# Optimization experiments

Measured on AMD Instinct MI355X. Metric: run time of the kernel, lower is better.

The kernel has to match this reference:

```python
import jax, jax.numpy as jnp
from jax import lax
import numpy as np

B, C, T = 128, 9, 512
M = 64                 # fourier modes
D_OB = 40
D_MODEL = C * D_OB     # 360
D_PE = 16
D = D_MODEL + D_PE     # 376
NHEAD = 4
DH = D // NHEAD        # 94
NHID = 2 * D_MODEL     # 720
NLAYERS = 3
FRAC = 0.5
MAX_PE = 100.0
EPS = 1e-5

def setup_inputs() -> dict:
    key = jax.random.key(0)
    ks = jax.random.split(key, 16)
    scale = 1.0 / (C * C)
    f32 = jnp.float32
    return {
        "x": jax.random.normal(ks[0], (B, C, T), f32),
        "w1r": scale * jax.random.uniform(ks[1], (C, C, M), f32),
        "w1i": scale * jax.random.uniform(ks[2], (C, C, M), f32),
        "conv_w": 0.1 * jax.random.normal(ks[3], (1, C, 3), f32),
        "bnf_g": jnp.ones((2 * M,), f32), "bnf_b": jnp.zeros((2 * M,), f32),
        "R_u": 1.0 + 0.02 * jax.random.normal(ks[4], (D_MODEL,), f32),
        "Wg1": 0.1 * jax.random.normal(ks[5], (D_OB, D_OB), f32),
        "Wg2": 0.1 * jax.random.normal(ks[6], (D_OB, D_OB), f32),
        "Wqkv": 0.02 * jax.random.normal(ks[7], (NLAYERS, D, 3 * D), f32),
        "bqkv": jnp.zeros((NLAYERS, 3 * D), f32),
        "Wo": 0.02 * jax.random.normal(ks[8], (NLAYERS, D, D), f32),
        "bo": jnp.zeros((NLAYERS, D), f32),
        "ln1g": jnp.ones((NLAYERS, D), f32), "ln1b": jnp.zeros((NLAYERS, D), f32),
        "W1": 0.02 * jax.random.normal(ks[9], (NLAYERS, D, NHID), f32),
        "b1": jnp.zeros((NLAYERS, NHID), f32),
        "W2": 0.02 * jax.random.normal(ks[10], (NLAYERS, NHID, D), f32),
        "b2": jnp.zeros((NLAYERS, D), f32),
        "ln2g": jnp.ones((NLAYERS, D), f32), "ln2b": jnp.zeros((NLAYERS, D), f32),
        "Wp": 0.02 * jax.random.normal(ks[11], (D, T), f32),
        "bp": jnp.zeros((T,), f32),
        "bnp_g": jnp.ones((T,), f32), "bnp_b": jnp.zeros((T,), f32),
    }

def _layernorm(z, g, b):
    m = z.mean(-1, keepdims=True)
    v = ((z - m) ** 2).mean(-1, keepdims=True)
    return (z - m) * lax.rsqrt(v + EPS) * g + b

def _batchnorm(z, g, b):  # training-mode BN over batch dim, z: [N, F]
    m = z.mean(0)
    v = ((z - m) ** 2).mean(0)
    return (z - m) * lax.rsqrt(v + EPS) * g + b

def _forward(x, w1r, w1i, conv_w, bnf_g, bnf_b, R_u, Wg1, Wg2,
             Wqkv, bqkv, Wo, bo, ln1g, ln1b, W1, b1, W2, b2, ln2g, ln2b,
             Wp, bp, bnp_g, bnp_b):
    # ---- SpectralConv1d (FrFT branch) ----
    xc = jnp.cos(x)                                   # [B,C,T]
    k = jnp.arange(T, dtype=jnp.float32)
    chirp = jnp.exp(-1j * jnp.pi * FRAC * k * k / T)  # FrFT chirp
    x_frft = jnp.fft.ifft(jnp.fft.fft(xc) * chirp)    # [B,C,T] complex
    w1 = (w1r + 1j * w1i).astype(jnp.complex64)
    out_modes = jnp.einsum('bix,iox->box', x_frft[:, :, :M], w1)   # [B,C,M]
    out_ft = jnp.concatenate([out_modes, jnp.zeros((B, C, T - M), jnp.complex64)], -1)
    ef = jnp.concatenate([jnp.abs(out_modes), jnp.angle(out_modes)], -1)  # [B,C,2M]
    # avg: Conv1d(C->1, k=3, pad=1, stride=1, no bias), then squeeze
    ef = lax.conv_general_dilated(ef, conv_w, window_strides=(1,), padding=((1, 1),),
                                  dimension_numbers=('NCH', 'OIH', 'NCH'))[:, 0, :]  # [B,2M]
    ef = jax.nn.relu(_batchnorm(ef, bnf_g, bnf_b))
    # ---- Raindrop branch ----
    src = jnp.transpose(x, (2, 0, 1))                 # [T,B,C]
    h = jnp.repeat(src, D_OB, axis=-1)                # repeat_interleave -> [T,B,d_model]
    h = jax.nn.relu(h * R_u)
    h4 = h.reshape(T, B, C, D_OB)
    adj = jnp.full((C, C), 1.0 / C, x.dtype)          # global_structure = ones, normalized
    h4 = jax.nn.relu(jnp.einsum('mn,tbnd,de->tbme', adj, h4, Wg1))
    h4 = jax.nn.relu(jnp.einsum('mn,tbnd,de->tbme', adj, h4, Wg2))
    h = h4.reshape(T, B, D_MODEL)
    # time positional encoding (PositionalEncodingTF, d_pe=16, MAX=100)
    times = jnp.broadcast_to(jnp.arange(T, dtype=jnp.float32)[:, None], (T, B))
    timescales = jnp.power(MAX_PE, jnp.linspace(0.0, 1.0, D_PE // 2))
    st = times[:, :, None] / timescales               # [T,B,8]
    pe = jnp.concatenate([jnp.sin(st), jnp.cos(st)], -1)  # [T,B,16]
    z = jnp.concatenate([h, pe], -1).transpose(1, 0, 2)   # [B,T,D]
    inv_sqrt_dh = 1.0 / np.sqrt(DH).astype(np.float32)
    for l in range(NLAYERS):
        qkv = z @ Wqkv[l] + bqkv[l]
        q, kk, v = jnp.split(qkv, 3, axis=-1)
        hd = lambda t: t.reshape(B, T, NHEAD, DH).transpose(0, 2, 1, 3)
        q, kk, v = hd(q), hd(kk), hd(v)
        att = jax.nn.softmax(jnp.einsum('bhqd,bhkd->bhqk', q, kk) * inv_sqrt_dh, axis=-1)
        o = jnp.einsum('bhqk,bhkd->bhqd', att, v).transpose(0, 2, 1, 3).reshape(B, T, D)
        z = _layernorm(z + o @ Wo[l] + bo[l], ln1g[l], ln1b[l])
        ff = jax.nn.relu(z @ W1[l] + b1[l]) @ W2[l] + b2[l]
        z = _layernorm(z + ff, ln2g[l], ln2b[l])
    et = z.mean(axis=1)                               # 'mean' aggregation -> [B,D]
    # projection: Linear(D, T) + ReLU + BatchNorm1d(T)
    et = _batchnorm(jax.nn.relu(et @ Wp + bp), bnp_g, bnp_b)  # [B,T]
    f = jnp.concatenate([ef, et], -1)                 # [B, 2M+T]
    fn = f / jnp.maximum(jnp.linalg.norm(f, axis=-1, keepdims=True), 1e-12)
    return fn, out_ft

def reference(x, w1r, w1i, conv_w, bnf_g, bnf_b, R_u, Wg1, Wg2,
              Wqkv, bqkv, Wo, bo, ln1g, ln1b, W1, b1, W2, b2, ln2g, ln2b,
              Wp, bp, bnp_g, bnp_b):
    return _forward(x, w1r, w1i, conv_w, bnf_g, bnf_b, R_u, Wg1, Wg2,
                    Wqkv, bqkv, Wo, bo, ln1g, ln1b, W1, b1, W2, b2, ln2g, ln2b,
                    Wp, bp, bnp_g, bnp_b)
```

## Files before the change

kernel.cpp:

```cpp
#include <hip/hip_runtime.h>
#include <math.h>

constexpr int cB = 128;
constexpr int cC = 9;
constexpr int cT = 512;
constexpr int cM = 64;
constexpr int cDOB = 40;
constexpr int cDM = 360;
constexpr int cD = 376;
constexpr int cDH = 94;
constexpr int cNHID = 720;
constexpr float cEPS = 1e-5f;
constexpr float cPI = 3.14159265358979323846f;

typedef __attribute__((ext_vector_type(8))) short short8b;
typedef __attribute__((ext_vector_type(4))) float f32x4;

__device__ __forceinline__ short f2b(float f) {
  union { float f; unsigned u; } c; c.f = f;
  unsigned r = (c.u + 0x7fffu + ((c.u >> 16) & 1u)) >> 16;
  return (short)r;
}
__device__ __forceinline__ float b2f(short h) {
  union { unsigned u; float f; } c; c.u = ((unsigned)(unsigned short)h) << 16;
  return c.f;
}

__global__ void k_chirp(float2* __restrict__ g) {
  int d = threadIdx.x;
  float re = 0.f, im = 0.f;
  for (int k = 0; k < cT; ++k) {
    int q = (k * k) & 2047;
    int p = (k * d) & 511;
    float th = cPI * ((float)p * (1.0f / 256.0f) - (float)q * (1.0f / 1024.0f));
    float s, c;
    sincosf(th, &s, &c);
    re += c; im += s;
  }
  g[d] = make_float2(re * (1.0f / 512.0f), im * (1.0f / 512.0f));
}

__global__ __launch_bounds__(512) void k_spectral(
    const float* __restrict__ x, const float* __restrict__ w1r,
    const float* __restrict__ w1i, const float2* __restrict__ g,
    float* __restrict__ outft, float* __restrict__ EF) {
  __shared__ float xc[cC][cT];
  __shared__ float2 gs[cT];
  __shared__ float2 xfr[cC][cM];
  int b = blockIdx.x, tid = threadIdx.x;
  for (int i = tid; i < cC * cT; i += 512)
    xc[i / cT][i % cT] = cosf(x[(size_t)b * cC * cT + i]);
  for (int i = tid; i < cT; i += 512) gs[i] = g[i];
  __syncthreads();
  for (int idx = tid; idx < cC * cM; idx += 512) {
    int c = idx / cM, m = idx % cM;
    float re = 0.f, im = 0.f;
    for (int t = 0; t < cT; ++t) {
      float xv = xc[c][t];
      float2 gv = gs[(m - t) & (cT - 1)];
      re += xv * gv.x; im += xv * gv.y;
    }
    xfr[c][m] = make_float2(re, im);
  }
  __syncthreads();
  for (int idx = tid; idx < cC * cM; idx += 512) {
    int o = idx / cM, m = idx % cM;
    float re = 0.f, im = 0.f;
    #pragma unroll
    for (int i = 0; i < cC; ++i) {
      float2 xv = xfr[i][m];
      float wr = w1r[(i * cC + o) * cM + m];
      float wi = w1i[(i * cC + o) * cM + m];
      re += xv.x * wr - xv.y * wi;
      im += xv.x * wi + xv.y * wr;
    }
    outft[(size_t)(b * cC + o) * cT + m] = re;
    EF[(b * cC + o) * (2 * cM) + m] = sqrtf(re * re + im * im);
    EF[(b * cC + o) * (2 * cM) + cM + m] = atan2f(im, re);
  }
  for (int idx = tid; idx < cC * (cT - cM); idx += 512) {
    int o = idx / (cT - cM);
    int r = idx % (cT - cM);
    outft[(size_t)(b * cC + o) * cT + cM + r] = 0.f;
  }
}

__global__ void k_convef(const float* __restrict__ EF, const float* __restrict__ cw,
                         float* __restrict__ efp) {
  int i = blockIdx.x * blockDim.x + threadIdx.x;
  if (i >= cB * 2 * cM) return;
  int b = i / (2 * cM), f = i % (2 * cM);
  float acc = 0.f;
  #pragma unroll
  for (int c = 0; c < cC; ++c) {
    const float* row = EF + (b * cC + c) * (2 * cM);
    if (f > 0) acc += row[f - 1] * cw[c * 3 + 0];
    acc += row[f] * cw[c * 3 + 1];
    if (f < 2 * cM - 1) acc += row[f + 1] * cw[c * 3 + 2];
  }
  efp[i] = acc;
}

__global__ __launch_bounds__(128) void k_bn(const float* __restrict__ in,
    const float* __restrict__ gam, const float* __restrict__ bet,
    float* __restrict__ dst, int F, int stride, int off, int reluAfter) {
  __shared__ float red[128];
  int f = blockIdx.x, bt = threadIdx.x;
  float v = in[(size_t)bt * F + f];
  red[bt] = v; __syncthreads();
  for (int s = 64; s > 0; s >>= 1) { if (bt < s) red[bt] += red[bt + s]; __syncthreads(); }
  float mean = red[0] * (1.0f / 128.0f);
  __syncthreads();
  float d = v - mean;
  red[bt] = d * d; __syncthreads();
  for (int s = 64; s > 0; s >>= 1) { if (bt < s) red[bt] += red[bt + s]; __syncthreads(); }
  float var = red[0] * (1.0f / 128.0f);
  float o = d * rsqrtf(var + cEPS) * gam[f] + bet[f];
  if (reluAfter) o = fmaxf(o, 0.f);
  dst[(size_t)bt * stride + off + f] = o;
}

__global__ __launch_bounds__(256) void k_raindrop(const float* __restrict__ x,
    const float* __restrict__ Ru, const float* __restrict__ Wg1,
    const float* __restrict__ Wg2, float* __restrict__ Z,
    short* __restrict__ Zb16, int bStart) {
  __shared__ float w1s[cDOB * cDOB], w2s[cDOB * cDOB], rus[cDM], tss[8];
  __shared__ float vsh[256][cDOB];
  int tid = threadIdx.x;
  for (int i = tid; i < cDOB * cDOB; i += 256) { w1s[i] = Wg1[i]; w2s[i] = Wg2[i]; }
  for (int i = tid; i < cDM; i += 256) rus[i] = Ru[i];
  if (tid < 8) tss[tid] = powf(100.0f, (float)tid * (1.0f / 7.0f));
  __syncthreads();
  int token0 = blockIdx.x * 256;
  int token = token0 + tid;
  int bl = token / cT, t = token % cT;
  int bg = bStart + bl;
  float s[cDOB];
  #pragma unroll
  for (int d = 0; d < cDOB; ++d) s[d] = 0.f;
  #pragma unroll
  for (int c = 0; c < cC; ++c) {
    float xv = x[((size_t)bg * cC + c) * cT + t];
    #pragma unroll
    for (int d = 0; d < cDOB; ++d) s[d] += fmaxf(xv * rus[c * cDOB + d], 0.f);
  }
  #pragma unroll
  for (int d = 0; d < cDOB; ++d) s[d] *= (1.0f / 9.0f);
  float u[cDOB];
  #pragma unroll
  for (int e = 0; e < cDOB; ++e) {
    float a = 0.f;
    #pragma unroll
    for (int d = 0; d < cDOB; ++d) a += s[d] * w1s[d * cDOB + e];
    u[e] = fmaxf(a, 0.f);
  }
  #pragma unroll
  for (int e = 0; e < cDOB; ++e) {
    float a = 0.f;
    #pragma unroll
    for (int d = 0; d < cDOB; ++d) a += u[d] * w2s[d * cDOB + e];
    vsh[tid][e] = fmaxf(a, 0.f);
  }
  __syncthreads();
  size_t zbase = (size_t)token0 * cD;
  for (int i = tid; i < 256 * cD; i += 256) {
    int tok = i / cD, col = i % cD;
    float val;
    if (col < cDM) {
      val = vsh[tok][col % cDOB];
    } else {
      int j = col - cDM;
      int tt = (token0 + tok) % cT;
      float st = (float)tt / tss[j & 7];
      val = (j < 8) ? sinf(st) : cosf(st);
    }
    Z[zbase + i] = val;
    Zb16[zbase + i] = f2b(val);
  }
}

__global__ __launch_bounds__(256) void k_cvtT(const float* __restrict__ in,
    short* __restrict__ out, int K, int N) {
  __shared__ float tile[32][33];
  int kb = blockIdx.x * 32, nb = blockIdx.y * 32;
  int tx = threadIdx.x & 31, ty = threadIdx.x >> 5;
  for (int i = ty; i < 32; i += 8) {
    int k = kb + i, n = nb + tx;
    tile[i][tx] = (k < K && n < N) ? in[(size_t)k * N + n] : 0.f;
  }
  __syncthreads();
  for (int i = ty; i < 32; i += 8) {
    int n = nb + i, k = kb + tx;
    if (n < N && k < K) out[(size_t)n * K + k] = f2b(tile[tx][i]);
  }
}

#define GEMM_CORE(EPILOGUE)                                                       \
  __shared__ short As[128][40];                                                   \
  __shared__ short Bs[128][40];                                                   \
  int tid = threadIdx.x;                                                          \
  int nbx = gridDim.x;                                                            \
  int flat = blockIdx.y * nbx + blockIdx.x;                                       \
  int nwg = nbx * gridDim.y;                                                      \
  int swz = ((nwg & 7) == 0) ? ((flat & 7) * (nwg >> 3) + (flat >> 3)) : flat;    \
  int m0 = (swz / nbx) * 128, n0 = (swz % nbx) * 128;                             \
  int w = tid >> 6, l = tid & 63;                                                 \
  int wm = w >> 1, wn = w & 1;                                                    \
  int lr = l & 15, lg = l >> 4;                                                   \
  f32x4 acc[4][4];                                                                \
  _Pragma("unroll") for (int i = 0; i < 4; ++i)                                   \
    _Pragma("unroll") for (int j = 0; j < 4; ++j)                                 \
      _Pragma("unroll") for (int r = 0; r < 4; ++r) acc[i][j][r] = 0.f;           \
  int srow = tid >> 1, skq = (tid & 1) << 4;                                      \
  int nK = (Kd + 31) >> 5;                                                        \
  for (int ks = 0; ks < nK; ++ks) {                                               \
    int k0 = ks << 5;                                                             \
    {                                                                             \
      int gm = m0 + srow;                                                         \
      int gk = k0 + skq;                                                          \
      short tmp[16];                                                              \
      const short* ap = At + (size_t)gm * Kd + gk;                                \
      _Pragma("unroll") for (int c = 0; c < 2; ++c) {                             \
        if (gm < Mr && gk + c * 8 + 7 < Kd) {                                     \
          *(short8b*)&tmp[c * 8] = *(const short8b*)(ap + c * 8);                 \
        } else {                                                                  \
          _Pragma("unroll") for (int j = 0; j < 8; ++j) tmp[c * 8 + j] = (short)0;\
        }                                                                         \
      }                                                                           \
      *(short8b*)&As[srow][skq]     = *(short8b*)&tmp[0];                         \
      *(short8b*)&As[srow][skq + 8] = *(short8b*)&tmp[8];                         \
    }                                                                             \
    {                                                                             \
      int gn = n0 + srow;                                                         \
      int gk = k0 + skq;                                                          \
      short tmp[16];                                                              \
      const short* bp = Bt + (size_t)gn * Kd + gk;                                \
      _Pragma("unroll") for (int c = 0; c < 2; ++c) {                             \
        if (gn < Nc && gk + c * 8 + 7 < Kd) {                                     \
          *(short8b*)&tmp[c * 8] = *(const short8b*)(bp + c * 8);                 \
        } else {                                                                  \
          _Pragma("unroll") for (int j = 0; j < 8; ++j) tmp[c * 8 + j] = (short)0;\
        }                                                                         \
      }                                                                           \
      *(short8b*)&Bs[srow][skq]     = *(short8b*)&tmp[0];                         \
      *(short8b*)&Bs[srow][skq + 8] = *(short8b*)&tmp[8];                         \
    }                                                                             \
    __syncthreads();                                                              \
    short8b af[4], bf[4];                                                         \
    _Pragma("unroll") for (int i = 0; i < 4; ++i)                                 \
      af[i] = *(short8b*)&As[wm * 64 + i * 16 + lr][lg * 8];                      \
    _Pragma("unroll") for (int j = 0; j < 4; ++j)                                 \
      bf[j] = *(short8b*)&Bs[wn * 64 + j * 16 + lr][lg * 8];                      \
    _Pragma("unroll") for (int i = 0; i < 4; ++i)                                 \
      _Pragma("unroll") for (int j = 0; j < 4; ++j)                               \
        acc[i][j] = __builtin_amdgcn_mfma_f32_16x16x32_bf16(af[i], bf[j], acc[i][j], 0, 0, 0); \
    __syncthreads();                                                              \
  }                                                                               \
  _Pragma("unroll") for (int i = 0; i < 4; ++i)                                   \
    _Pragma("unroll") for (int j = 0; j < 4; ++j) {                               \
      int gn = n0 + wn * 64 + j * 16 + lr;                                        \
      if (gn >= Nc) continue;                                                     \
      float bv = bias ? bias[gn] : 0.f;                                           \
      int gmb = m0 + wm * 64 + i * 16 + lg * 4;                                   \
      _Pragma("unroll") for (int r = 0; r < 4; ++r) {                             \
        int gm = gmb + r;                                                         \
        if (gm >= Mr) continue;                                                   \
        float vv = acc[i][j][r] + bv;                                             \
        EPILOGUE                                                                  \
      }                                                                           \
    }

__global__ __launch_bounds__(256) void k_gemm_mfma2(
    const short* __restrict__ At, const short* __restrict__ Bt,
    const float* __restrict__ bias, float* __restrict__ Cm,
    int Mr, int Nc, int Kd, int relu) {
  GEMM_CORE({
    if (relu) vv = fmaxf(vv, 0.f);
    Cm[(size_t)gm * Nc + gn] = vv;
  })
}

__global__ __launch_bounds__(256) void k_gemm_b16(
    const short* __restrict__ At, const short* __restrict__ Bt,
    const float* __restrict__ bias, short* __restrict__ Cm,
    int Mr, int Nc, int Kd, int relu) {
  GEMM_CORE({
    if (relu) vv = fmaxf(vv, 0.f);
    Cm[(size_t)gm * Nc + gn] = f2b(vv);
  })
}

__global__ __launch_bounds__(256) void k_gemm_qkv(
    const short* __restrict__ At, const short* __restrict__ Bt,
    const float* __restrict__ bias, unsigned* __restrict__ Cp,
    int Mr, int Nc, int Kd) {
  GEMM_CORE({
    short hv = f2b(vv);
    short lv2 = f2b(vv - b2f(hv));
    Cp[(size_t)gm * Nc + gn] =
        ((unsigned)(unsigned short)hv) | (((unsigned)(unsigned short)lv2) << 16);
  })
}

__global__ __launch_bounds__(256) void k_gemm(const float* __restrict__ A,
    const float* __restrict__ Bm, const float* __restrict__ bias,
    float* __restrict__ Cm, int Mr, int Nc, int Kd, int relu) {
  __shared__ float As[16][68];
  __shared__ float Bs[16][68];
  int tid = threadIdx.x;
  int tx = tid & 15, ty = tid >> 4;
  int n0 = blockIdx.x * 64, m0 = blockIdx.y * 64;
  float acc[4][4] = {{0.f}};
  for (int k0 = 0; k0 < Kd; k0 += 16) {
    {
      int row = tid >> 2, kq = (tid & 3) << 2;
      int gm = m0 + row, gk = k0 + kq;
      float4 av = make_float4(0.f, 0.f, 0.f, 0.f);
      if (gm < Mr) {
        const float* ap = A + (size_t)gm * Kd + gk;
        if (gk + 3 < Kd) av = *(const float4*)ap;
        else {
          if (gk + 0 < Kd) av.x = ap[0];
          if (gk + 1 < Kd) av.y = ap[1];
          if (gk + 2 < Kd) av.z = ap[2];
        }
      }
      As[kq + 0][row] = av.x; As[kq + 1][row] = av.y;
      As[kq + 2][row] = av.z; As[kq + 3][row] = av.w;
    }
    {
      int kr = tid >> 4, nc = (tid & 15) << 2;
      int gk = k0 + kr, gn = n0 + nc;
      float4 bv = make_float4(0.f, 0.f, 0.f, 0.f);
      if (gk < Kd && gn < Nc) {
        const float* bp = Bm + (size_t)gk * Nc + gn;
        if (gn + 3 < Nc) bv = *(const float4*)bp;
        else {
          bv.x = bp[0];
          if (gn + 1 < Nc) bv.y = bp[1];
          if (gn + 2 < Nc) bv.z = bp[2];
        }
      }
      *(float4*)&Bs[kr][nc] = bv;
    }
    __syncthreads();
    #pragma unroll
    for (int k = 0; k < 16; ++k) {
      float4 a = *(const float4*)&As[k][ty << 2];
      float4 b = *(const float4*)&Bs[k][tx << 2];
      acc[0][0] += a.x * b.x; acc[0][1] += a.x * b.y; acc[0][2] += a.x * b.z; acc[0][3] += a.x * b.w;
      acc[1][0] += a.y * b.x; acc[1][1] += a.y * b.y; acc[1][2] += a.y * b.z; acc[1][3] += a.y * b.w;
      acc[2][0] += a.z * b.x; acc[2][1] += a.z * b.y; acc[2][2] += a.z * b.z; acc[2][3] += a.z * b.w;
      acc[3][0] += a.w * b.x; acc[3][1] += a.w * b.y; acc[3][2] += a.w * b.z; acc[3][3] += a.w * b.w;
    }
    __syncthreads();
  }
  #pragma unroll
  for (int i = 0; i < 4; ++i) {
    int gm = m0 + (ty << 2) + i;
    if (gm >= Mr) continue;
    #pragma unroll
    for (int j = 0; j < 4; ++j) {
      int gn = n0 + (tx << 2) + j;
      if (gn >= Nc) continue;
      float v = acc[i][j] + (bias ? bias[gn] : 0.f);
      if (relu) v = fmaxf(v, 0.f);
      Cm[(size_t)gm * Nc + gn] = v;
    }
  }
}

__global__ __launch_bounds__(512) void k_attn_mfma2(const unsigned* __restrict__ Qp,
    short* __restrict__ ATT16) {
  __shared__ __align__(16) char raw[62464];
  short* kv_h = (short*)raw;
  short* kv_l = (short*)(raw + 12288);
  int tid = threadIdx.x;
  int w = tid >> 6, l = tid & 63;
  int lr = l & 15, lg = l >> 4;
  short* p_h = (short*)(raw + 24576) + w * 16 * 72;
  short* p_l = (short*)(raw + 43008) + w * 16 * 72;
  float* fs_w = (float*)(raw + 61440) + w * 16;
  float* il_w = (float*)(raw + 61952) + w * 16;
  int qb = blockIdx.x, h = blockIdx.y, bl = blockIdx.z;
  size_t tokBase = (size_t)bl * cT;
  const float scale = 0.103142125f;
  int qrow = w * 16 + lr;

  short8b qh_s[3], ql_s[3];
  #pragma unroll
  for (int ph = 0; ph < 2; ++ph) {
    size_t base = (tokBase + qb * 128 + ph * 64) * 1128ull + h * cDH;
    for (int task = tid; task < 768; task += 512) {
      int oct = task >> 6, tok = task & 63;
      size_t src = base + (size_t)tok * 1128 + oct * 8;
      uint4 a = *(const uint4*)(Qp + src);
      uint4 b = *(const uint4*)(Qp + src + 4);
      unsigned p[8] = {a.x, a.y, a.z, a.w, b.x, b.y, b.z, b.w};
      short hv[8], lv[8];
      #pragma unroll
      for (int i = 0; i < 8; ++i) { hv[i] = (short)(p[i] & 0xffffu); lv[i] = (short)(p[i] >> 16); }
      if (oct == 11) { hv[6] = 0; hv[7] = 0; lv[6] = 0; lv[7] = 0; }
      int dst = (oct * 64 + (tok ^ (oct & 7))) * 8;
      *(short8b*)&kv_h[dst] = *(short8b*)hv;
      *(short8b*)&kv_l[dst] = *(short8b*)lv;
    }
    __syncthreads();
    if ((w >> 2) == ph) {
      int tokl = qrow & 63;
      #pragma unroll
      for (int s = 0; s < 3; ++s) {
        int o = s * 4 + lg;
        int src = (o * 64 + (tokl ^ (o & 7))) * 8;
        qh_s[s] = *(short8b*)&kv_h[src];
        ql_s[s] = *(short8b*)&kv_l[src];
      }
    }
    __syncthreads();
  }

  f32x4 of[6];
  #pragma unroll
  for (int f = 0; f < 6; ++f)
    #pragma unroll
    for (int r = 0; r < 4; ++r) of[f][r] = 0.f;
  float mrow[4], lrow[4];
  #pragma unroll
  for (int r = 0; r < 4; ++r) { mrow[r] = -1e30f; lrow[r] = 0.f; }

  for (int kt = 0; kt < 8; ++kt) {
    __syncthreads();
    {
      size_t base = (tokBase + kt * 64) * 1128ull + cD + h * cDH;
      for (int task = tid; task < 768; task += 512) {
        int oct = task >> 6, tok = task & 63;
        size_t src = base + (size_t)tok * 1128 + oct * 8;
        uint4 a = *(const uint4*)(Qp + src);
        uint4 b = *(const uint4*)(Qp + src + 4);
        unsigned p[8] = {a.x, a.y, a.z, a.w, b.x, b.y, b.z, b.w};
        short hv[8], lv[8];
        #pragma unroll
        for (int i = 0; i < 8; ++i) { hv[i] = (short)(p[i] & 0xffffu); lv[i] = (short)(p[i] >> 16); }
        if (oct == 11) { hv[6] = 0; hv[7] = 0; lv[6] = 0; lv[7] = 0; }
        int dst = (oct * 64 + (tok ^ (oct & 7))) * 8;
        *(short8b*)&kv_h[dst] = *(short8b*)hv;
        *(short8b*)&kv_l[dst] = *(short8b*)lv;
      }
    }
    __syncthreads();
    f32x4 sf4[4];
    #pragma unroll
    for (int j = 0; j < 4; ++j)
      #pragma unroll
      for (int r = 0; r < 4; ++r) sf4[j][r] = 0.f;
    #pragma unroll
    for (int j = 0; j < 4; ++j) {
      #pragma unroll
      for (int s = 0; s < 3; ++s) {
        int o = s * 4 + lg;
        int src = (o * 64 + ((j * 16 + lr) ^ (o & 7))) * 8;
        short8b bh = *(short8b*)&kv_h[src];
        short8b bl2 = *(short8b*)&kv_l[src];
        sf4[j] = __builtin_amdgcn_mfma_f32_16x16x32_bf16(qh_s[s], bh, sf4[j], 0, 0, 0);
        sf4[j] = __builtin_amdgcn_mfma_f32_16x16x32_bf16(ql_s[s], bh, sf4[j], 0, 0, 0);
        sf4[j] = __builtin_amdgcn_mfma_f32_16x16x32_bf16(qh_s[s], bl2, sf4[j], 0, 0, 0);
      }
    }
    float fscv[4];
    #pragma unroll
    for (int r = 0; r < 4; ++r) {
      float s0 = sf4[0][r] * scale, s1 = sf4[1][r] * scale;
      float s2 = sf4[2][r] * scale, s3 = sf4[3][r] * scale;
      float mx = fmaxf(fmaxf(s0, s1), fmaxf(s2, s3));
      for (int off = 8; off > 0; off >>= 1) mx = fmaxf(mx, __shfl_xor(mx, off, 16));
      float mnew = fmaxf(mrow[r], mx);
      float fsc = __expf(mrow[r] - mnew);
      float p0 = __expf(s0 - mnew), p1 = __expf(s1 - mnew);
      float p2 = __expf(s2 - mnew), p3 = __expf(s3 - mnew);
      float ps = p0 + p1 + p2 + p3;
      for (int off = 8; off > 0; off >>= 1) ps += __shfl_xor(ps, off, 16);
      lrow[r] = lrow[r] * fsc + ps;
      mrow[r] = mnew;
      fscv[r] = fsc;
      int row = (lg * 4 + r) * 72;
      short h0 = f2b(p0);
      p_h[row + 0 * 16 + lr] = h0; p_l[row + 0 * 16 + lr] = f2b(p0 - b2f(h0));
      short h1 = f2b(p1);
      p_h[row + 1 * 16 + lr] = h1; p_l[row + 1 * 16 + lr] = f2b(p1 - b2f(h1));
      short h2 = f2b(p2);
      p_h[row + 2 * 16 + lr] = h2; p_l[row + 2 * 16 + lr] = f2b(p2 - b2f(h2));
      short h3 = f2b(p3);
      p_h[row + 3 * 16 + lr] = h3; p_l[row + 3 * 16 + lr] = f2b(p3 - b2f(h3));
    }
    if (lr == 0) {
      #pragma unroll
      for (int r = 0; r < 4; ++r) fs_w[lg * 4 + r] = fscv[r];
    }
    __syncthreads();
    {
      size_t base = (tokBase + kt * 64) * 1128ull + 2 * cD + h * cDH;
      for (int task = tid; task < 768; task += 512) {
        int d = task % 96, t8 = task / 96;
        short hv[8], lv[8];
        if (d < cDH) {
          #pragma unroll
          for (int i = 0; i < 8; ++i) {
            unsigned p = Qp[base + (size_t)(t8 * 8 + i) * 1128 + d];
            hv[i] = (short)(p & 0xffffu); lv[i] = (short)(p >> 16);
          }
        } else {
          #pragma unroll
          for (int i = 0; i < 8; ++i) { hv[i] = 0; lv[i] = 0; }
        }
        int dst = d * 64 + ((t8 * 8) ^ ((d & 7) << 3));
        *(short8b*)&kv_h[dst] = *(short8b*)hv;
        *(short8b*)&kv_l[dst] = *(short8b*)lv;
      }
    }
    __syncthreads();
    float fs = fs_w[lr];
    #pragma unroll
    for (int f = 0; f < 6; ++f)
      #pragma unroll
      for (int r = 0; r < 4; ++r) of[f][r] *= fs;
    #pragma unroll
    for (int s = 0; s < 2; ++s) {
      int pof = lr * 72 + s * 32 + lg * 8;
      short8b ph = *(short8b*)&p_h[pof];
      short8b pl = *(short8b*)&p_l[pof];
      #pragma unroll
      for (int f = 0; f < 6; ++f) {
        int d = f * 16 + lr;
        int vof = d * 64 + ((s * 32 + lg * 8) ^ ((d & 7) << 3));
        short8b vh = *(short8b*)&kv_h[vof];
        short8b vl = *(short8b*)&kv_l[vof];
        of[f] = __builtin_amdgcn_mfma_f32_16x16x32_bf16(vh, ph, of[f], 0, 0, 0);
        of[f] = __builtin_amdgcn_mfma_f32_16x16x32_bf16(vl, ph, of[f], 0, 0, 0);
        of[f] = __builtin_amdgcn_mfma_f32_16x16x32_bf16(vh, pl, of[f], 0, 0, 0);
      }
    }
  }
  if (lr == 0) {
    #pragma unroll
    for (int r = 0; r < 4; ++r) il_w[lg * 4 + r] = 1.0f / lrow[r];
  }
  __syncthreads();
  float il = il_w[lr];
  float* obuf = (float*)raw;
  #pragma unroll
  for (int f = 0; f < 6; ++f) {
    #pragma unroll
    for (int r = 0; r < 4; ++r) {
      int d = f * 16 + lg * 4 + r;
      if (d < cDH) obuf[(w * 16 + lr) * 98 + d] = of[f][r] * il;
    }
  }
  __syncthreads();
  for (int idx = tid; idx < 128 * cDH; idx += 512) {
    int q = idx / cDH, d = idx % cDH;
    ATT16[(tokBase + qb * 128 + q) * (size_t)cD + h * cDH + d] = f2b(obuf[q * 98 + d]);
  }
}

__global__ __launch_bounds__(256) void k_addln(float* __restrict__ Z,
    const float* __restrict__ Y, const float* __restrict__ gam,
    const float* __restrict__ bet, short* __restrict__ Zb16) {
  int wid = threadIdx.x >> 6, lane = threadIdx.x & 63;
  size_t base = ((size_t)blockIdx.x * 4 + wid) * cD;
  float v[6];
  float sum = 0.f;
  #pragma unroll
  for (int j = 0; j < 6; ++j) {
    int c = lane + j * 64;
    float t = 0.f;
    if (c < cD) t = Z[base + c] + Y[base + c];
    v[j] = t; sum += t;
  }
  #pragma unroll
  for (int off = 32; off > 0; off >>= 1) sum += __shfl_xor(sum, off, 64);
  float mean = sum / (float)cD;
  float vs = 0.f;
  #pragma unroll
  for (int j = 0; j < 6; ++j) {
    int c = lane + j * 64;
    if (c < cD) { float d = v[j] - mean; vs += d * d; }
  }
  #pragma unroll
  for (int off = 32; off > 0; off >>= 1) vs += __shfl_xor(vs, off, 64);
  float inv = rsqrtf(vs / (float)cD + cEPS);
  #pragma unroll
  for (int j = 0; j < 6; ++j) {
    int c = lane + j * 64;
    if (c < cD) {
      float res = (v[j] - mean) * inv * gam[c] + bet[c];
      Z[base + c] = res;
      Zb16[base + c] = f2b(res);
    }
  }
}

__global__ __launch_bounds__(384) void k_meant(const float* __restrict__ Z,
    float* __restrict__ et, int bStart) {
  int bl = blockIdx.x, d = threadIdx.x;
  if (d >= cD) return;
  float s = 0.f;
  for (int t = 0; t < cT; ++t) s += Z[((size_t)bl * cT + t) * cD + d];
  et[(size_t)(bStart + bl) * cD + d] = s * (1.0f / 512.0f);
}

__global__ __launch_bounds__(128) void k_final(const float* __restrict__ fst,
    float* __restrict__ out) {
  __shared__ float red[128];
  int b = blockIdx.x, tid = threadIdx.x;
  float v[5]; float ss = 0.f;
  #pragma unroll
  for (int i = 0; i < 5; ++i) {
    v[i] = fst[(size_t)b * 640 + tid + i * 128];
    ss += v[i] * v[i];
  }
  red[tid] = ss; __syncthreads();
  for (int s = 64; s > 0; s >>= 1) { if (tid < s) red[tid] += red[tid + s]; __syncthreads(); }
  float inv = 1.0f / fmaxf(sqrtf(red[0]), 1e-12f);
  #pragma unroll
  for (int i = 0; i < 5; ++i) out[(size_t)b * 640 + tid + i * 128] = v[i] * inv;
}

extern "C" void kernel_launch(void* const* d_in, const int* in_sizes, int n_in,
                              void* d_out, int out_size, void* d_ws, size_t ws_size,
                              hipStream_t stream) {
  (void)in_sizes; (void)n_in; (void)out_size;
  const float* x     = (const float*)d_in[0];
  const float* w1r   = (const float*)d_in[1];
  const float* w1i   = (const float*)d_in[2];
  const float* convw = (const float*)d_in[3];
  const float* bnfg  = (const float*)d_in[4];
  const float* bnfb  = (const float*)d_in[5];
  const float* Ru    = (const float*)d_in[6];
  const float* Wg1   = (const float*)d_in[7];
  const float* Wg2   = (const float*)d_in[8];
  const float* Wqkv  = (const float*)d_in[9];
  const float* bqkv  = (const float*)d_in[10];
  const float* Wo    = (const float*)d_in[11];
  const float* bo    = (const float*)d_in[12];
  const float* ln1g  = (const float*)d_in[13];
  const float* ln1b  = (const float*)d_in[14];
  const float* W1    = (const float*)d_in[15];
  const float* b1    = (const float*)d_in[16];
  const float* W2    = (const float*)d_in[17];
  const float* b2    = (const float*)d_in[18];
  const float* ln2g  = (const float*)d_in[19];
  const float* ln2b  = (const float*)d_in[20];
  const float* Wp    = (const float*)d_in[21];
  const float* bp    = (const float*)d_in[22];
  const float* bnpg  = (const float*)d_in[23];
  const float* bnpb  = (const float*)d_in[24];

  float* W = (float*)d_ws;
  size_t wsFloats = ws_size / 4;
  float* fst = W;
  float* et  = fst + 81920;
  float* etp = et + 48128;
  float2* g  = (float2*)(etp + 65536);
  float* EF  = (float*)g + 1024;
  float* efp = EF + 147456;
  short* bfw = (short*)(efp + 16384);
  const size_t bfwFloats = 1660416;
  const size_t fixedFloats = 81920 + 48128 + 65536 + 1024 + 147456 + 16384 + bfwFloats;

  const size_t oQKV = 0;
  const size_t oWO  = oQKV + (size_t)3 * 1128 * 376;
  const size_t oW1  = oWO  + (size_t)3 * 376 * 376;
  const size_t oW2  = oW1  + (size_t)3 * 720 * 376;

  float* outF  = (float*)d_out;
  float* outft = outF + cB * 640;

  if (wsFloats < fixedFloats) return;

  int Bc = 0;
  float* chunk = nullptr;
  for (int c = 128; c >= 1; c >>= 1) {
    size_t need = (size_t)c * cT * 1880 + 64;
    if (fixedFloats + need <= wsFloats) { Bc = c; chunk = W + fixedFloats; break; }
  }
  bool haveChunk = (Bc > 0);

  if (haveChunk) {
    for (int l = 0; l < 3; ++l) {
      k_cvtT<<<dim3(12, 36), 256, 0, stream>>>(Wqkv + (size_t)l * cD * 1128,
          bfw + oQKV + (size_t)l * 1128 * 376, cD, 1128);
      k_cvtT<<<dim3(12, 12), 256, 0, stream>>>(Wo + (size_t)l * cD * cD,
          bfw + oWO + (size_t)l * 376 * 376, cD, cD);
      k_cvtT<<<dim3(12, 23), 256, 0, stream>>>(W1 + (size_t)l * cD * cNHID,
          bfw + oW1 + (size_t)l * 720 * 376, cD, cNHID);
      k_cvtT<<<dim3(23, 12), 256, 0, stream>>>(W2 + (size_t)l * cNHID * cD,
          bfw + oW2 + (size_t)l * 376 * 720, cNHID, cD);
    }

    float* Zb      = chunk;
    short* Zb16    = (short*)(Zb + (size_t)Bc * cT * cD);
    unsigned* QKVp = (unsigned*)(Zb16 + (size_t)Bc * cT * cD);
    short* ATT16   = (short*)(QKVp + (size_t)Bc * cT * 1128);
    for (int b0 = 0; b0 < cB; b0 += Bc) {
      int ntok = Bc * cT;
      int mt = (ntok + 127) / 128;
      short* Hb16  = (short*)QKVp;
      float* WoOut = (float*)(Hb16 + (size_t)ntok * 720);
      float* FF2o  = WoOut + (size_t)ntok * 376;
      k_raindrop<<<ntok / 256, 256, 0, stream>>>(x, Ru, Wg1, Wg2, Zb, Zb16, b0);
      for (int l = 0; l < 3; ++l) {
        k_gemm_qkv<<<dim3(9, mt), 256, 0, stream>>>(
            Zb16, bfw + oQKV + (size_t)l * 1128 * 376,
            bqkv + (size_t)l * 1128, QKVp, ntok, 1128, cD);
        k_attn_mfma2<<<dim3(4, 4, Bc), 512, 0, stream>>>(QKVp, ATT16);
        k_gemm_mfma2<<<dim3(3, mt), 256, 0, stream>>>(
            ATT16, bfw + oWO + (size_t)l * 376 * 376,
            bo + (size_t)l * cD, WoOut, ntok, cD, cD, 0);
        k_addln<<<ntok / 4, 256, 0, stream>>>(Zb, WoOut, ln1g + l * cD, ln1b + l * cD, Zb16);
        k_gemm_b16<<<dim3(6, mt), 256, 0, stream>>>(
            Zb16, bfw + oW1 + (size_t)l * 720 * 376,
            b1 + (size_t)l * cNHID, Hb16, ntok, cNHID, cD, 1);
        k_gemm_mfma2<<<dim3(3, mt), 256, 0, stream>>>(
            Hb16, bfw + oW2 + (size_t)l * 376 * 720,
            b2 + (size_t)l * cD, FF2o, ntok, cD, cNHID, 0);
        k_addln<<<ntok / 4, 256, 0, stream>>>(Zb, FF2o, ln2g + l * cD, ln2b + l * cD, Zb16);
      }
      k_meant<<<Bc, 384, 0, stream>>>(Zb, et, b0);
    }
    k_gemm<<<dim3(cT / 64, cB / 64), 256, 0, stream>>>(et, Wp, bp, etp, cB, cT, cD, 1);
  }

  k_chirp<<<1, 512, 0, stream>>>(g);
  k_spectral<<<cB, 512, 0, stream>>>(x, w1r, w1i, g, outft, EF);
  k_convef<<<(cB * 2 * cM + 255) / 256, 256, 0, stream>>>(EF, convw, efp);
  k_bn<<<2 * cM, 128, 0, stream>>>(efp, bnfg, bnfb, fst, 2 * cM, 640, 0, 1);

  if (haveChunk)
    k_bn<<<cT, 128, 0, stream>>>(etp, bnpg, bnpb, fst, cT, 640, 2 * cM, 0);

  k_final<<<cB, 128, 0, stream>>>(fst, outF);
}
```

Before: 2.875 ms.

## Pad GEMM operands to multiples of 32 and stage tiles with direct global-to-LDS loads

Pads the bf16 activations and transposed weights along K to 384 and 736 with zero columns, so the GEMM loop can drop its bounds checks. Global tiles are now copied straight into LDS with global_load_lds, using an XOR-swizzled unpadded layout to avoid bank conflicts. Producers (raindrop, attention, addln, FFN1 epilogue) write the zero padding explicitly. The aim is fewer VGPR round trips and fewer instructions per tile load. The cost is a slightly larger workspace, extra padding writes, and reliance on M and N tile edges staying in bounds, since the row checks were removed from the loads.

```diff
diff --git a/kernel.cpp b/kernel.cpp
--- a/kernel.cpp
+++ b/kernel.cpp
@@ -8,13 +8,17 @@
 constexpr int cDOB = 40;
 constexpr int cDM = 360;
 constexpr int cD = 376;
+constexpr int cDP = 384;
 constexpr int cDH = 94;
 constexpr int cNHID = 720;
+constexpr int cNHP = 736;
 constexpr float cEPS = 1e-5f;
 constexpr float cPI = 3.14159265358979323846f;
 
 typedef __attribute__((ext_vector_type(8))) short short8b;
 typedef __attribute__((ext_vector_type(4))) float f32x4;
+typedef const __attribute__((address_space(1))) short glb_short;
+typedef __attribute__((address_space(3))) short lds_short;
 
 __device__ __forceinline__ short f2b(float f) {
   union { float f; unsigned u; } c; c.f = f;
@@ -175,12 +179,16 @@
       val = (j < 8) ? sinf(st) : cosf(st);
     }
     Z[zbase + i] = val;
-    Zb16[zbase + i] = f2b(val);
+    Zb16[(size_t)(token0 + tok) * cDP + col] = f2b(val);
+  }
+  for (int i = tid; i < 256 * 8; i += 256) {
+    int tok = i >> 3, c = cD + (i & 7);
+    Zb16[(size_t)(token0 + tok) * cDP + c] = 0;
   }
 }
 
 __global__ __launch_bounds__(256) void k_cvtT(const float* __restrict__ in,
-    short* __restrict__ out, int K, int N) {
+    short* __restrict__ out, int K, int N, int Kpad) {
   __shared__ float tile[32][33];
   int kb = blockIdx.x * 32, nb = blockIdx.y * 32;
   int tx = threadIdx.x & 31, ty = threadIdx.x >> 5;
@@ -191,13 +199,13 @@
   __syncthreads();
   for (int i = ty; i < 32; i += 8) {
     int n = nb + i, k = kb + tx;
-    if (n < N && k < K) out[(size_t)n * K + k] = f2b(tile[tx][i]);
+    if (n < N && k < Kpad) out[(size_t)n * Kpad + k] = f2b(tile[tx][i]);
   }
 }
 
 #define GEMM_CORE(EPILOGUE)                                                       \
-  __shared__ short As[128][40];                                                   \
-  __shared__ short Bs[128][40];                                                   \
+  __shared__ __align__(16) short As[128 * 32];                                    \
+  __shared__ __align__(16) short Bs[128 * 32];                                    \
   int tid = threadIdx.x;                                                          \
   int nbx = gridDim.x;                                                            \
   int flat = blockIdx.y * nbx + blockIdx.x;                                       \
@@ -211,46 +219,33 @@
   _Pragma("unroll") for (int i = 0; i < 4; ++i)                                   \
     _Pragma("unroll") for (int j = 0; j < 4; ++j)                                 \
       _Pragma("unroll") for (int r = 0; r < 4; ++r) acc[i][j][r] = 0.f;           \
-  int srow = tid >> 1, skq = (tid & 1) << 4;                                      \
-  int nK = (Kd + 31) >> 5;                                                        \
+  int rbase = w * 32;                                                             \
+  int lrow = l >> 2, lslot = l & 3;                                               \
+  int nK = Kd >> 5;                                                               \
   for (int ks = 0; ks < nK; ++ks) {                                               \
     int k0 = ks << 5;                                                             \
-    {                                                                             \
-      int gm = m0 + srow;                                                         \
-      int gk = k0 + skq;                                                          \
-      short tmp[16];                                                              \
-      const short* ap = At + (size_t)gm * Kd + gk;                                \
-      _Pragma("unroll") for (int c = 0; c < 2; ++c) {                             \
-        if (gm < Mr && gk + c * 8 + 7 < Kd) {                                     \
-          *(short8b*)&tmp[c * 8] = *(const short8b*)(ap + c * 8);                 \
-        } else {                                                                  \
-          _Pragma("unroll") for (int j = 0; j < 8; ++j) tmp[c * 8 + j] = (short)0;\
-        }                                                                         \
-      }                                                                           \
-      *(short8b*)&As[srow][skq]     = *(short8b*)&tmp[0];                         \
-      *(short8b*)&As[srow][skq + 8] = *(short8b*)&tmp[8];                         \
-    }                                                                             \
-    {                                                                             \
-      int gn = n0 + srow;                                                         \
-      int gk = k0 + skq;                                                          \
-      short tmp[16];                                                              \
-      const short* bp = Bt + (size_t)gn * Kd + gk;                                \
-      _Pragma("unroll") for (int c = 0; c < 2; ++c) {                             \
-        if (gn < Nc && gk + c * 8 + 7 < Kd) {                                     \
-          *(short8b*)&tmp[c * 8] = *(const short8b*)(bp + c * 8);                 \
-        } else {                                                                  \
-          _Pragma("unroll") for (int j = 0; j < 8; ++j) tmp[c * 8 + j] = (short)0;\
-        }                                                                         \
-      }                                                                           \
-      *(short8b*)&Bs[srow][skq]     = *(short8b*)&tmp[0];                         \
-      *(short8b*)&Bs[srow][skq + 8] = *(short8b*)&tmp[8];                         \
+    _Pragma("unroll") for (int q = 0; q < 2; ++q) {                               \
+      int r = rbase + q * 16 + lrow;                                              \
+      int cl = lslot ^ ((r >> 1) & 3);                                            \
+      __builtin_amdgcn_global_load_lds(                                           \
+          (glb_short*)(At + (size_t)(m0 + r) * Kd + k0 + cl * 8),                 \
+          (lds_short*)&As[(rbase + q * 16) * 32], 16, 0, 0);                      \
+      __builtin_amdgcn_global_load_lds(                                           \
+          (glb_short*)(Bt + (size_t)(n0 + r) * Kd + k0 + cl * 8),                 \
+          (lds_short*)&Bs[(rbase + q * 16) * 32], 16, 0, 0);                      \
     }                                                                             \
     __syncthreads();                                                              \
     short8b af[4], bf[4];                                                         \
-    _Pragma("unroll") for (int i = 0; i < 4; ++i)                                 \
-      af[i] = *(short8b*)&As[wm * 64 + i * 16 + lr][lg * 8];                      \
-    _Pragma("unroll") for (int j = 0; j < 4; ++j)                                 \
-      bf[j] = *(short8b*)&Bs[wn * 64 + j * 16 + lr][lg * 8];                      \
+    _Pragma("unroll") for (int i = 0; i < 4; ++i) {                               \
+      int row = wm * 64 + i * 16 + lr;                                            \
+      int sl = lg ^ ((row >> 1) & 3);                                             \
+      af[i] = *(short8b*)&As[row * 32 + sl * 8];                                  \
+    }                                                                             \
+    _Pragma("unroll") for (int j = 0; j < 4; ++j) {                               \
+      int row = wn * 64 + j * 16 + lr;                                            \
+      int sl = lg ^ ((row >> 1) & 3);                                             \
+      bf[j] = *(short8b*)&Bs[row * 32 + sl * 8];                                  \
+    }                                                                             \
     _Pragma("unroll") for (int i = 0; i < 4; ++i)                                 \
       _Pragma("unroll") for (int j = 0; j < 4; ++j)                               \
         acc[i][j] = __builtin_amdgcn_mfma_f32_16x16x32_bf16(af[i], bf[j], acc[i][j], 0, 0, 0); \
@@ -259,8 +254,8 @@
   _Pragma("unroll") for (int i = 0; i < 4; ++i)                                   \
     _Pragma("unroll") for (int j = 0; j < 4; ++j) {                               \
       int gn = n0 + wn * 64 + j * 16 + lr;                                        \
-      if (gn >= Nc) continue;                                                     \
-      float bv = bias ? bias[gn] : 0.f;                                           \
+      if (gn >= Nst) continue;                                                    \
+      float bv = (bias && gn < Nc) ? bias[gn] : 0.f;                              \
       int gmb = m0 + wm * 64 + i * 16 + lg * 4;                                   \
       _Pragma("unroll") for (int r = 0; r < 4; ++r) {                             \
         int gm = gmb + r;                                                         \
@@ -273,31 +268,31 @@
 __global__ __launch_bounds__(256) void k_gemm_mfma2(
     const short* __restrict__ At, const short* __restrict__ Bt,
     const float* __restrict__ bias, float* __restrict__ Cm,
-    int Mr, int Nc, int Kd, int relu) {
+    int Mr, int Nc, int Nst, int Kd, int relu) {
   GEMM_CORE({
     if (relu) vv = fmaxf(vv, 0.f);
-    Cm[(size_t)gm * Nc + gn] = vv;
+    Cm[(size_t)gm * Nst + gn] = vv;
   })
 }
 
 __global__ __launch_bounds__(256) void k_gemm_b16(
     const short* __restrict__ At, const short* __restrict__ Bt,
     const float* __restrict__ bias, short* __restrict__ Cm,
-    int Mr, int Nc, int Kd, int relu) {
+    int Mr, int Nc, int Nst, int Kd, int relu) {
   GEMM_CORE({
     if (relu) vv = fmaxf(vv, 0.f);
-    Cm[(size_t)gm * Nc + gn] = f2b(vv);
+    Cm[(size_t)gm * Nst + gn] = (gn < Nc) ? f2b(vv) : (short)0;
   })
 }
 
 __global__ __launch_bounds__(256) void k_gemm_qkv(
     const short* __restrict__ At, const short* __restrict__ Bt,
     const float* __restrict__ bias, unsigned* __restrict__ Cp,
-    int Mr, int Nc, int Kd) {
+    int Mr, int Nc, int Nst, int Kd) {
   GEMM_CORE({
     short hv = f2b(vv);
     short lv2 = f2b(vv - b2f(hv));
-    Cp[(size_t)gm * Nc + gn] =
+    Cp[(size_t)gm * Nst + gn] =
         ((unsigned)(unsigned short)hv) | (((unsigned)(unsigned short)lv2) << 16);
   })
 }
@@ -558,7 +553,13 @@
   __syncthreads();
   for (int idx = tid; idx < 128 * cDH; idx += 512) {
     int q = idx / cDH, d = idx % cDH;
-    ATT16[(tokBase + qb * 128 + q) * (size_t)cD + h * cDH + d] = f2b(obuf[q * 98 + d]);
+    ATT16[(tokBase + qb * 128 + q) * (size_t)cDP + h * cDH + d] = f2b(obuf[q * 98 + d]);
+  }
+  if (h == 3) {
+    for (int idx = tid; idx < 128 * 8; idx += 512) {
+      int q = idx >> 3, c = cD + (idx & 7);
+      ATT16[(tokBase + qb * 128 + q) * (size_t)cDP + c] = 0;
+    }
   }
 }
 
@@ -566,7 +567,9 @@
     const float* __restrict__ Y, const float* __restrict__ gam,
     const float* __restrict__ bet, short* __restrict__ Zb16) {
   int wid = threadIdx.x >> 6, lane = threadIdx.x & 63;
-  size_t base = ((size_t)blockIdx.x * 4 + wid) * cD;
+  size_t token = (size_t)blockIdx.x * 4 + wid;
+  size_t base = token * cD;
+  size_t b16 = token * cDP;
   float v[6];
   float sum = 0.f;
   #pragma unroll
@@ -594,7 +597,9 @@
     if (c < cD) {
       float res = (v[j] - mean) * inv * gam[c] + bet[c];
       Z[base + c] = res;
-      Zb16[base + c] = f2b(res);
+      Zb16[b16 + c] = f2b(res);
+    } else if (c < cDP) {
+      Zb16[b16 + c] = 0;
     }
   }
 }
@@ -664,13 +669,13 @@
   float* EF  = (float*)g + 1024;
   float* efp = EF + 147456;
   short* bfw = (short*)(efp + 16384);
-  const size_t bfwFloats = 1660416;
+  const size_t oQKV = 0;
+  const size_t oWO  = oQKV + (size_t)3 * 1128 * cDP;
+  const size_t oW1  = oWO  + (size_t)3 * 376 * cDP;
+  const size_t oW2  = oW1  + (size_t)3 * 720 * cDP;
+  const size_t bfwShorts = oW2 + (size_t)3 * 376 * cNHP;
+  const size_t bfwFloats = (bfwShorts + 1) / 2;
   const size_t fixedFloats = 81920 + 48128 + 65536 + 1024 + 147456 + 16384 + bfwFloats;
-
-  const size_t oQKV = 0;
-  const size_t oWO  = oQKV + (size_t)3 * 1128 * 376;
-  const size_t oW1  = oWO  + (size_t)3 * 376 * 376;
-  const size_t oW2  = oW1  + (size_t)3 * 720 * 376;
 
   float* outF  = (float*)d_out;
   float* outft = outF + cB * 640;
@@ -680,7 +685,7 @@
   int Bc = 0;
   float* chunk = nullptr;
   for (int c = 128; c >= 1; c >>= 1) {
-    size_t need = (size_t)c * cT * 1880 + 64;
+    size_t need = (size_t)c * cT * 1888 + 64;
     if (fixedFloats + need <= wsFloats) { Bc = c; chunk = W + fixedFloats; break; }
   }
   bool haveChunk = (Bc > 0);
@@ -688,41 +693,41 @@
   if (haveChunk) {
     for (int l = 0; l < 3; ++l) {
       k_cvtT<<<dim3(12, 36), 256, 0, stream>>>(Wqkv + (size_t)l * cD * 1128,
-          bfw + oQKV + (size_t)l * 1128 * 376, cD, 1128);
+          bfw + oQKV + (size_t)l * 1128 * cDP, cD, 1128, cDP);
       k_cvtT<<<dim3(12, 12), 256, 0, stream>>>(Wo + (size_t)l * cD * cD,
-          bfw + oWO + (size_t)l * 376 * 376, cD, cD);
+          bfw + oWO + (size_t)l * 376 * cDP, cD, cD, cDP);
       k_cvtT<<<dim3(12, 23), 256, 0, stream>>>(W1 + (size_t)l * cD * cNHID,
-          bfw + oW1 + (size_t)l * 720 * 376, cD, cNHID);
+          bfw + oW1 + (size_t)l * 720 * cDP, cD, cNHID, cDP);
       k_cvtT<<<dim3(23, 12), 256, 0, stream>>>(W2 + (size_t)l * cNHID * cD,
-          bfw + oW2 + (size_t)l * 376 * 720, cNHID, cD);
+          bfw + oW2 + (size_t)l * 376 * cNHP, cNHID, cD, cNHP);
     }
 
     float* Zb      = chunk;
     short* Zb16    = (short*)(Zb + (size_t)Bc * cT * cD);
-    unsigned* QKVp = (unsigned*)(Zb16 + (size_t)Bc * cT * cD);
+    unsigned* QKVp = (unsigned*)(Zb16 + (size_t)Bc * cT * cDP);
     short* ATT16   = (short*)(QKVp + (size_t)Bc * cT * 1128);
     for (int b0 = 0; b0 < cB; b0 += Bc) {
       int ntok = Bc * cT;
       int mt = (ntok + 127) / 128;
       short* Hb16  = (short*)QKVp;
-      float* WoOut = (float*)(Hb16 + (size_t)ntok * 720);
+      float* WoOut = (float*)(Hb16 + (size_t)ntok * cNHP);
       float* FF2o  = WoOut + (size_t)ntok * 376;
       k_raindrop<<<ntok / 256, 256, 0, stream>>>(x, Ru, Wg1, Wg2, Zb, Zb16, b0);
       for (int l = 0; l < 3; ++l) {
         k_gemm_qkv<<<dim3(9, mt), 256, 0, stream>>>(
-            Zb16, bfw + oQKV + (size_t)l * 1128 * 376,
-            bqkv + (size_t)l * 1128, QKVp, ntok, 1128, cD);
+            Zb16, bfw + oQKV + (size_t)l * 1128 * cDP,
+            bqkv + (size_t)l * 1128, QKVp, ntok, 1128, 1128, cDP);
         k_attn_mfma2<<<dim3(4, 4, Bc), 512, 0, stream>>>(QKVp, ATT16);
         k_gemm_mfma2<<<dim3(3, mt), 256, 0, stream>>>(
-            ATT16, bfw + oWO + (size_t)l * 376 * 376,
-            bo + (size_t)l * cD, WoOut, ntok, cD, cD, 0);
+            ATT16, bfw + oWO + (size_t)l * 376 * cDP,
+            bo + (size_t)l * cD, WoOut, ntok, cD, cD, cDP, 0);
         k_addln<<<ntok / 4, 256, 0, stream>>>(Zb, WoOut, ln1g + l * cD, ln1b + l * cD, Zb16);
         k_gemm_b16<<<dim3(6, mt), 256, 0, stream>>>(
-            Zb16, bfw + oW1 + (size_t)l * 720 * 376,
-            b1 + (size_t)l * cNHID, Hb16, ntok, cNHID, cD, 1);
+            Zb16, bfw + oW1 + (size_t)l * 720 * cDP,
+            b1 + (size_t)l * cNHID, Hb16, ntok, cNHID, cNHP, cDP, 1);
         k_gemm_mfma2<<<dim3(3, mt), 256, 0, stream>>>(
-            Hb16, bfw + oW2 + (size_t)l * 376 * 720,
-            b2 + (size_t)l * cD, FF2o, ntok, cD, cNHID, 0);
+            Hb16, bfw + oW2 + (size_t)l * 376 * cNHP,
+            b2 + (size_t)l * cD, FF2o, ntok, cD, cD, cNHP, 0);
         k_addln<<<ntok / 4, 256, 0, stream>>>(Zb, FF2o, ln2g + l * cD, ln2b + l * cD, Zb16);
       }
       k_meant<<<Bc, 384, 0, stream>>>(Zb, et, b0);
```

After: 2.651 ms, median of 2. 1.08x faster.
